# Kernel tuning notes

Measured on AMD Instinct MI355X. Metric: run time of the kernel, lower is better.

The kernel has to match this reference:

```python
import jax, jax.numpy as jnp
import numpy as np
from jax import lax

B, T, E = 2, 2048, 2048
H, D = 16, 128
C = H * D          # qk_dim == v_dim == 2048
K = 4              # short conv kernel size
EPS = 1e-5


def setup_inputs() -> dict:
    key = jax.random.key(0)
    ks = jax.random.split(key, 11)
    s = 0.02
    return {
        "x": jax.random.normal(ks[0], (B, T, E), dtype=jnp.float32),
        "recurrent_state": jnp.zeros((B, H, D, D), dtype=jnp.float32),
        "Wq": jax.random.normal(ks[1], (C, E), dtype=jnp.float32) * s,
        "Wk": jax.random.normal(ks[2], (C, E), dtype=jnp.float32) * s,
        "Wv": jax.random.normal(ks[3], (C, E), dtype=jnp.float32) * s,
        "Wbeta": jax.random.normal(ks[4], (H, E), dtype=jnp.float32) * s,
        "Wgate": jax.random.normal(ks[5], (C, E), dtype=jnp.float32) * s,
        "Wo": jax.random.normal(ks[6], (E, C), dtype=jnp.float32) * s,
        "wq_conv": jax.random.normal(ks[7], (C, 1, K), dtype=jnp.float32) * 0.5,
        "wk_conv": jax.random.normal(ks[8], (C, 1, K), dtype=jnp.float32) * 0.5,
        "wv_conv": jax.random.normal(ks[9], (C, 1, K), dtype=jnp.float32) * 0.5,
    }


def _causal_dwconv(u, w):
    # u: (B, T, C), w: (C, 1, K). Torch pads both sides by K-1 then truncates
    # to length T -> equivalent to causal left-pad of K-1.
    u = u.transpose(0, 2, 1)  # (B, C, T)
    y = lax.conv_general_dilated(
        u, w, window_strides=(1,), padding=[(K - 1, 0)],
        feature_group_count=C, dimension_numbers=("NCH", "OIH", "NCH"))
    return y.transpose(0, 2, 1)  # (B, T, C)


def _delta_scan(q, k, v, beta, state):
    # q,k,v: (B,T,H,D); beta: (B,T,H); state: (B,H,D,D)
    def step(S, inp):
        qt, kt, vt, bt = inp  # (B,H,D),(B,H,D),(B,H,D),(B,H)
        b = bt[..., None, None]
        S = (1.0 - b) * S + b * (kt[..., :, None] * vt[..., None, :])  # bhde
        o = jnp.einsum("bhde,bhd->bhe", S, qt)
        return S, o

    xs = (q.transpose(1, 0, 2, 3), k.transpose(1, 0, 2, 3),
          v.transpose(1, 0, 2, 3), beta.transpose(1, 0, 2))
    final_state, outs = lax.scan(step, state, xs)
    return outs.transpose(1, 0, 2, 3), final_state  # (B,T,H,D)


def reference(x, recurrent_state, Wq, Wk, Wv, Wbeta, Wgate, Wo,
              wq_conv, wk_conv, wv_conv):
    q = jax.nn.silu(_causal_dwconv(x @ Wq.T, wq_conv))
    k = jax.nn.silu(_causal_dwconv(x @ Wk.T, wk_conv))
    v = jax.nn.silu(_causal_dwconv(x @ Wv.T, wv_conv))
    beta = jax.nn.sigmoid(x @ Wbeta.T)   # (B,T,H)
    gate = jax.nn.sigmoid(x @ Wgate.T)   # (B,T,C)

    q = q.reshape(B, T, H, D) * (D ** -0.5)
    k = k.reshape(B, T, H, D)
    v = v.reshape(B, T, H, D)

    out, new_state = _delta_scan(q, k, v, beta, recurrent_state)  # (B,T,H,D)

    # GroupNorm(num_groups=H, channels=C, affine=False) over (B, C, T):
    # normalizes each (batch, head) group over its (D, T) elements.
    mean = out.mean(axis=(1, 3), keepdims=True)
    var = out.var(axis=(1, 3), keepdims=True)
    out = (out - mean) * lax.rsqrt(var + EPS)

    out = out.reshape(B, T, C) * gate
    y = out @ Wo.T  # (B,T,E)
    return y, new_state
```

## Files before the change

### kernel.cpp

```cpp
#include <hip/hip_runtime.h>
#include <hip/hip_bf16.h>
#include <math.h>

#define BB 2
#define TT 2048
#define EE 2048
#define HH 16
#define DD 128
#define CC 2048
#define KCONV 4
#define CHUNK 128
#define NC 16
#define GN_EPS 1e-5f

typedef __bf16 bf16x8 __attribute__((ext_vector_type(8)));
typedef __bf16 bf16x4 __attribute__((ext_vector_type(4)));
typedef float  f32x4  __attribute__((ext_vector_type(4)));

#define GLD16(gp, lp)                                                          \
  __builtin_amdgcn_global_load_lds(                                            \
      (const __attribute__((address_space(1))) void*)(gp),                     \
      (__attribute__((address_space(3))) void*)(lp), 16, 0, 0)

__device__ __forceinline__ bf16x8 ldfrag(const __bf16* buf, int row, int kg)
{
  return *(const bf16x8*)(buf + row * 128 + ((kg ^ (row & 7)) << 3));
}

__global__ __launch_bounds__(256)
void convert_w(const float* __restrict__ Wq, const float* __restrict__ Wk,
               const float* __restrict__ Wv, const float* __restrict__ Wg,
               const float* __restrict__ Wo, __bf16* __restrict__ Wcat,
               __bf16* __restrict__ Wob)
{
  const int i = (blockIdx.x * 256 + threadIdx.x) * 4;
  const int WN = 4194304;
  const float* src;
  __bf16* dst;
  int off;
  if (i < 4 * WN) {
    const int seg = i >> 22;
    src = seg == 0 ? Wq : seg == 1 ? Wk : seg == 2 ? Wv : Wg;
    dst = Wcat + ((size_t)seg << 22);
    off = i & (WN - 1);
  } else { src = Wo; dst = Wob; off = i - 4 * WN; }
  const float4 v = *(const float4*)(src + off);
  bf16x4 o;
  o[0] = (__bf16)v.x; o[1] = (__bf16)v.y; o[2] = (__bf16)v.z; o[3] = (__bf16)v.w;
  *(bf16x4*)(dst + off) = o;
}

__global__ __launch_bounds__(256)
void beta_ker(const float* __restrict__ x, const float* __restrict__ Wb,
              float* __restrict__ betab, __bf16* __restrict__ xbf)
{
  __shared__ float wsb[16 * 1024];
  const int tid = threadIdx.x;
  const int w = tid >> 6, lane = tid & 63;
  const int row = blockIdx.x * 4 + w;
  const float* xrow = x + (size_t)row * EE;
  __bf16* xbrow = xbf + (size_t)row * EE;

  float acc[16] = {};
#pragma unroll
  for (int kt = 0; kt < 2; ++kt) {
    __syncthreads();
#pragma unroll
    for (int it = 0; it < 16; ++it) {
      const int i = tid + it * 256;
      const int h = i >> 8, kq = i & 255;
      *(float4*)&wsb[h * 1024 + kq * 4] =
          *(const float4*)(Wb + (size_t)h * EE + kt * 1024 + kq * 4);
    }
    __syncthreads();
#pragma unroll
    for (int j = 0; j < 4; ++j) {
      const int kof = lane * 4 + j * 256;
      const float4 xv = *(const float4*)(xrow + kt * 1024 + kof);
      bf16x4 xb;
      xb[0] = (__bf16)xv.x; xb[1] = (__bf16)xv.y;
      xb[2] = (__bf16)xv.z; xb[3] = (__bf16)xv.w;
      *(bf16x4*)(xbrow + kt * 1024 + kof) = xb;
#pragma unroll
      for (int h = 0; h < 16; ++h) {
        const float4 wv = *(const float4*)&wsb[h * 1024 + kof];
        acc[h] += xv.x * wv.x + xv.y * wv.y + xv.z * wv.z + xv.w * wv.w;
      }
    }
  }
#pragma unroll
  for (int h = 0; h < 16; ++h) {
#pragma unroll
    for (int off = 32; off; off >>= 1)
      acc[h] += __shfl_xor(acc[h], off, 64);
  }
#pragma unroll
  for (int h = 0; h < 16; ++h)
    if (lane == h)
      betab[(size_t)row * HH + h] = 1.f / (1.f + expf(-acc[h]));
}

__global__ __launch_bounds__(512)
void gemm_big(const __bf16* __restrict__ A, const __bf16* __restrict__ Bm,
              __bf16* __restrict__ o0, __bf16* __restrict__ o1,
              __bf16* __restrict__ o2, __bf16* __restrict__ o3)
{
  __shared__ __attribute__((aligned(16))) unsigned char smem[163840];
  __bf16 (*ldsA)[256 * 64] = (__bf16(*)[256 * 64])smem;
  __bf16 (*ldsB)[256 * 64] = (__bf16(*)[256 * 64])(smem + 98304);

  const int tid = threadIdx.x;
  const int w = tid >> 6, l = tid & 63;
  const int wm = w >> 2, wn = w & 3;
  const int orig = blockIdx.x + (blockIdx.y << 5);
  const int swz = (orig & 7) * 64 + (orig >> 3);
  const int m0 = (swz & 15) * 256, n0 = (swz >> 4) * 256;
  const int NT = EE / 64;

  const int sr0 = w * 8 + (l >> 3);
  const int skg = l & 7;
  const int fr = l & 15;
  const int fkg = l >> 4;

#define STAGE_A(tile, half) do {                                               \
    const int b_ = (tile) % 3;                                                 \
    const int r0_ = sr0;                                                       \
    const int r1_ = 64 + sr0;                                                  \
    GLD16(A + (size_t)(m0 + (half) * 128 + r0_) * 2048 + (tile) * 64           \
              + ((skg ^ (r0_ & 7)) << 3),                                      \
          ldsA[b_] + ((half) * 128 + w * 8) * 64);                             \
    GLD16(A + (size_t)(m0 + (half) * 128 + r1_) * 2048 + (tile) * 64           \
              + ((skg ^ (r1_ & 7)) << 3),                                      \
          ldsA[b_] + ((half) * 128 + 64 + w * 8) * 64);                        \
  } while (0)

#define STAGE_B(tile, half) do {                                               \
    const int b_ = (tile) & 1;                                                 \
    const int r0_ = sr0;                                                       \
    const int r1_ = 64 + sr0;                                                  \
    GLD16(Bm + (size_t)(n0 + (half) * 128 + r0_) * 2048 + (tile) * 64          \
              + ((skg ^ (r0_ & 7)) << 3),                                      \
          ldsB[b_] + ((half) * 128 + w * 8) * 64);                             \
    GLD16(Bm + (size_t)(n0 + (half) * 128 + r1_) * 2048 + (tile) * 64          \
              + ((skg ^ (r1_ & 7)) << 3),                                      \
          ldsB[b_] + ((half) * 128 + 64 + w * 8) * 64);                        \
  } while (0)

#define LDA_FRAG(dst, ab, q, mf, ks) do {                                      \
    const int row_ = wm * 128 + (q) * 32 + (mf) * 16 + fr;                     \
    const int kg_ = (ks) * 4 + fkg;                                            \
    dst = *(const bf16x8*)&ldsA[ab][row_ * 64 + ((kg_ ^ (row_ & 7)) << 3)];    \
  } while (0)
#define LDB_FRAG(dst, bb, nf, ks) do {                                         \
    const int row_ = wn * 64 + (nf) * 16 + fr;                                 \
    const int kg_ = (ks) * 4 + fkg;                                            \
    dst = *(const bf16x8*)&ldsB[bb][row_ * 64 + ((kg_ ^ (row_ & 7)) << 3)];    \
  } while (0)

  f32x4 acc[8][4] = {};

  STAGE_A(0, 0); STAGE_A(0, 1); STAGE_B(0, 0); STAGE_B(0, 1);
  STAGE_A(1, 0); STAGE_A(1, 1); STAGE_B(1, 0);
  asm volatile("s_waitcnt vmcnt(6)" ::: "memory");
  __builtin_amdgcn_s_barrier();

  for (int t = 0; t < NT; ++t) {
    const int abuf = t % 3;
    const int bbuf = t & 1;
    bf16x8 bfr[4][2];

    {
      bf16x8 af[2][2];
#pragma unroll
      for (int nf = 0; nf < 4; ++nf)
#pragma unroll
        for (int ks = 0; ks < 2; ++ks) LDB_FRAG(bfr[nf][ks], bbuf, nf, ks);
#pragma unroll
      for (int mf = 0; mf < 2; ++mf)
#pragma unroll
        for (int ks = 0; ks < 2; ++ks) LDA_FRAG(af[mf][ks], abuf, 0, mf, ks);
      if (t + 1 < NT) STAGE_B(t + 1, 1);
      __builtin_amdgcn_s_barrier();
      __builtin_amdgcn_s_setprio(1);
#pragma unroll
      for (int mf = 0; mf < 2; ++mf)
#pragma unroll
        for (int nf = 0; nf < 4; ++nf)
#pragma unroll
          for (int ks = 0; ks < 2; ++ks)
            acc[mf][nf] = __builtin_amdgcn_mfma_f32_16x16x32_bf16(
                af[mf][ks], bfr[nf][ks], acc[mf][nf], 0, 0, 0);
      __builtin_amdgcn_s_setprio(0);
    }

#pragma unroll
    for (int q = 1; q < 4; ++q) {
      bf16x8 af[2][2];
#pragma unroll
      for (int mf = 0; mf < 2; ++mf)
#pragma unroll
        for (int ks = 0; ks < 2; ++ks) LDA_FRAG(af[mf][ks], abuf, q, mf, ks);
      if (q == 1) {
        if (t + 2 < NT) STAGE_A(t + 2, 0);
      } else if (q == 2) {
        if (t + 2 < NT) STAGE_A(t + 2, 1);
      } else {
        if (t + 2 < NT) STAGE_B(t + 2, 0);
        if (t == NT - 2)     asm volatile("s_waitcnt vmcnt(0)" ::: "memory");
        else if (t < NT - 2) asm volatile("s_waitcnt vmcnt(6)" ::: "memory");
      }
      __builtin_amdgcn_s_barrier();
      __builtin_amdgcn_s_setprio(1);
#pragma unroll
      for (int mf = 0; mf < 2; ++mf)
#pragma unroll
        for (int nf = 0; nf < 4; ++nf)
#pragma unroll
          for (int ks = 0; ks < 2; ++ks)
            acc[2 * q + mf][nf] = __builtin_amdgcn_mfma_f32_16x16x32_bf16(
                af[mf][ks], bfr[nf][ks], acc[2 * q + mf][nf], 0, 0, 0);
      __builtin_amdgcn_s_setprio(0);
    }
  }

  __syncthreads();
  const int proj = n0 >> 11;
  const int nb = n0 & 2047;
  __bf16* outp = proj == 0 ? o0 : proj == 1 ? o1 : proj == 2 ? o2 : o3;
  __bf16* ep = (__bf16*)smem + (size_t)w * 9216;
  const int crow = (l >> 4) * 4;
#pragma unroll
  for (int mf2 = 0; mf2 < 8; ++mf2)
#pragma unroll
    for (int nf = 0; nf < 4; ++nf)
#pragma unroll
      for (int r = 0; r < 4; ++r) {
        const int row = mf2 * 16 + crow + r;
        float vv = acc[mf2][nf][r];
        if (proj == 3) vv = 1.f / (1.f + expf(-vv));
        ep[row * 72 + nf * 16 + fr] = (__bf16)vv;
      }
#pragma unroll
  for (int it = 0; it < 16; ++it) {
    const int row = it * 8 + (l >> 3);
    const int c8 = (l & 7) * 8;
    const bf16x8 v8 = *(const bf16x8*)&ep[row * 72 + c8];
    *(bf16x8*)(outp + (size_t)(m0 + wm * 128 + row) * 2048 + nb + wn * 64 + c8) = v8;
  }
#undef STAGE_A
#undef STAGE_B
#undef LDA_FRAG
#undef LDB_FRAG
}

__global__ __launch_bounds__(512)
void gemm_wo(const __bf16* __restrict__ A, const __bf16* __restrict__ Bm,
             float* __restrict__ Cm)
{
  __shared__ __attribute__((aligned(16))) unsigned char smem[147456];
  __bf16 (*ldsA)[128 * 64] = (__bf16(*)[128 * 64])smem;
  __bf16 (*ldsB)[256 * 64] = (__bf16(*)[256 * 64])(smem + 49152);

  const int tid = threadIdx.x;
  const int w = tid >> 6, l = tid & 63;
  const int wm = w >> 2, wn = w & 3;
  const int orig = blockIdx.x + (blockIdx.y << 3);
  const int swz = (orig & 7) * 32 + (orig >> 3);
  const int m0 = (swz & 31) * 128, n0 = (swz >> 5) * 256;
  const int NT = CC / 64;

  const int sr0 = w * 8 + (l >> 3);
  const int skg = l & 7;
  const int fr = l & 15;
  const int fkg = l >> 4;

#define STAGE_AW(tile) do {                                                    \
    const int b_ = (tile) % 3;                                                 \
    const int r0_ = sr0;                                                       \
    const int r1_ = 64 + sr0;                                                  \
    GLD16(A + (size_t)(m0 + r0_) * 2048 + (tile) * 64                          \
              + ((skg ^ (r0_ & 7)) << 3),                                      \
          ldsA[b_] + (w * 8) * 64);                                            \
    GLD16(A + (size_t)(m0 + r1_) * 2048 + (tile) * 64                          \
              + ((skg ^ (r1_ & 7)) << 3),                                      \
          ldsA[b_] + (64 + w * 8) * 64);                                       \
  } while (0)

#define STAGE_BW(tile, half) do {                                              \
    const int b_ = (tile) % 3;                                                 \
    const int r0_ = sr0;                                                       \
    const int r1_ = 64 + sr0;                                                  \
    GLD16(Bm + (size_t)(n0 + (half) * 128 + r0_) * 2048 + (tile) * 64          \
              + ((skg ^ (r0_ & 7)) << 3),                                      \
          ldsB[b_] + ((half) * 128 + w * 8) * 64);                             \
    GLD16(Bm + (size_t)(n0 + (half) * 128 + r1_) * 2048 + (tile) * 64          \
              + ((skg ^ (r1_ & 7)) << 3),                                      \
          ldsB[b_] + ((half) * 128 + 64 + w * 8) * 64);                        \
  } while (0)

#define LDA_FRAGW(dst, ab, mf, ks) do {                                        \
    const int row_ = wm * 64 + (mf) * 16 + fr;                                 \
    const int kg_ = (ks) * 4 + fkg;                                            \
    dst = *(const bf16x8*)&ldsA[ab][row_ * 64 + ((kg_ ^ (row_ & 7)) << 3)];    \
  } while (0)
#define LDB_FRAGW(dst, bb, nf, ks) do {                                        \
    const int row_ = wn * 64 + (nf) * 16 + fr;                                 \
    const int kg_ = (ks) * 4 + fkg;                                            \
    dst = *(const bf16x8*)&ldsB[bb][row_ * 64 + ((kg_ ^ (row_ & 7)) << 3)];    \
  } while (0)

  f32x4 acc[4][4] = {};

  STAGE_BW(0, 0); STAGE_BW(0, 1); STAGE_AW(0);
  STAGE_BW(1, 0); STAGE_BW(1, 1); STAGE_AW(1);

  for (int t = 0; t < NT; ++t) {
    const int buf = t % 3;
    bf16x8 bfr[4][2];
    bf16x8 af[4][2];

    if (t == NT - 1) asm volatile("s_waitcnt vmcnt(0)" ::: "memory");
    else             asm volatile("s_waitcnt vmcnt(6)" ::: "memory");
    __builtin_amdgcn_s_barrier();

#pragma unroll
    for (int nf = 0; nf < 4; ++nf)
#pragma unroll
      for (int ks = 0; ks < 2; ++ks) LDB_FRAGW(bfr[nf][ks], buf, nf, ks);
#pragma unroll
    for (int mf = 0; mf < 4; ++mf)
#pragma unroll
      for (int ks = 0; ks < 2; ++ks) LDA_FRAGW(af[mf][ks], buf, mf, ks);

    if (t + 2 < NT) { STAGE_BW(t + 2, 0); STAGE_BW(t + 2, 1); STAGE_AW(t + 2); }

    __builtin_amdgcn_s_setprio(1);
#pragma unroll
    for (int mf = 0; mf < 4; ++mf)
#pragma unroll
      for (int nf = 0; nf < 4; ++nf)
#pragma unroll
        for (int ks = 0; ks < 2; ++ks)
          acc[mf][nf] = __builtin_amdgcn_mfma_f32_16x16x32_bf16(
              af[mf][ks], bfr[nf][ks], acc[mf][nf], 0, 0, 0);
    __builtin_amdgcn_s_setprio(0);
  }

  __syncthreads();
  float* ep = (float*)smem + (size_t)w * (64 * 68);
  const int crow = (l >> 4) * 4;
#pragma unroll
  for (int mf = 0; mf < 4; ++mf)
#pragma unroll
    for (int nf = 0; nf < 4; ++nf)
#pragma unroll
      for (int r = 0; r < 4; ++r)
        ep[(mf * 16 + crow + r) * 68 + nf * 16 + fr] = acc[mf][nf][r];
#pragma unroll
  for (int it = 0; it < 16; ++it) {
    const int row = it * 4 + (l >> 4);
    const int c4 = (l & 15) * 4;
    const float4 v4 = *(const float4*)&ep[row * 68 + c4];
    *(float4*)(Cm + (size_t)(m0 + wm * 64 + row) * 2048 + n0 + wn * 64 + c4) = v4;
  }
#undef STAGE_AW
#undef STAGE_BW
#undef LDA_FRAGW
#undef LDB_FRAGW
}

__global__ __launch_bounds__(256)
void conv_tr(const __bf16* __restrict__ u_q, const __bf16* __restrict__ u_k,
             const __bf16* __restrict__ u_v, const float* __restrict__ wq,
             const float* __restrict__ wk, const float* __restrict__ wv,
             __bf16* __restrict__ qbf, __bf16* __restrict__ kbf,
             __bf16* __restrict__ kT, __bf16* __restrict__ vT, float qscale)
{
  const int t0 = blockIdx.x * 64, c0 = blockIdx.y * 64;
  const int which = blockIdx.z / BB, b = blockIdx.z % BB;
  const __bf16* u = which == 0 ? u_q : which == 1 ? u_k : u_v;
  const float* wc = which == 0 ? wq : which == 1 ? wk : wv;
  const float scale = which == 0 ? qscale : 1.f;
  const int tid = threadIdx.x;
  __shared__ __attribute__((aligned(16))) __bf16 tile[64][72];

#pragma unroll
  for (int it = 0; it < 2; ++it) {
    const int idx = tid + it * 256;
    const int tl = idx >> 3, g = idx & 7;
    const int t = t0 + tl;
    const int c8 = c0 + g * 8;
    const size_t base = ((size_t)(b * TT + t)) * CC + c8;
    const bf16x8 z = {};
    const bf16x8 uu0 = *(const bf16x8*)(u + base);
    const bf16x8 uu1 = (t >= 1) ? *(const bf16x8*)(u + base - CC)     : z;
    const bf16x8 uu2 = (t >= 2) ? *(const bf16x8*)(u + base - 2 * CC) : z;
    const bf16x8 uu3 = (t >= 3) ? *(const bf16x8*)(u + base - 3 * CC) : z;
    bf16x8 o;
#pragma unroll
    for (int jj = 0; jj < 8; ++jj) {
      const float4 wv4 = *(const float4*)(wc + (size_t)(c8 + jj) * 4);
      const float vv = wv4.x * (float)uu3[jj] + wv4.y * (float)uu2[jj]
                     + wv4.z * (float)uu1[jj] + wv4.w * (float)uu0[jj];
      o[jj] = (__bf16)(vv / (1.f + expf(-vv)) * scale);
    }
    if (which == 0) *(bf16x8*)(qbf + base) = o;
    if (which == 1) *(bf16x8*)(kbf + base) = o;
    if (which >= 1) *(bf16x8*)&tile[tl][g * 8] = o;
  }
  if (which >= 1) {
    __syncthreads();
    const int h = c0 >> 7, d0 = c0 & 127;
    const int bh = b * HH + h;
    __bf16* dst = (which == 1) ? kT : vT;
#pragma unroll
    for (int it = 0; it < 2; ++it) {
      const int idx = tid + it * 256;
      const int dl = idx >> 3, g = idx & 7;
      bf16x8 o;
#pragma unroll
      for (int jj = 0; jj < 8; ++jj) o[jj] = tile[g * 8 + jj][dl];
      *(bf16x8*)(dst + ((size_t)(bh * DD + d0 + dl)) * TT + t0 + g * 8) = o;
    }
  }
}

__global__ __launch_bounds__(256)
void phaseA_mfma(const __bf16* __restrict__ kT, const __bf16* __restrict__ vT,
                 const float* __restrict__ beta, float* __restrict__ contribT,
                 float* __restrict__ decay)
{
  const int c = blockIdx.x, h = blockIdx.y, b = blockIdx.z;
  const int bh = b * HH + h;
  const int tid = threadIdx.x;
  const int w = tid >> 6, lane = tid & 63;
  const int wm = w >> 1, wn = w & 1;

  __shared__ __attribute__((aligned(16))) __bf16 bufVT[128 * 128];
  __shared__ __attribute__((aligned(16))) __bf16 bufKW[128 * 128];
  __shared__ float lc[CHUNK], bsh[CHUNK], wgt[CHUNK];

  {
    const __bf16* vbase = vT + ((size_t)bh * DD) * TT + c * CHUNK;
#pragma unroll
    for (int jj = 0; jj < 8; ++jj) {
      const int row = w * 32 + jj * 4 + (lane >> 4);
      const int g = lane & 15;
      GLD16(vbase + (size_t)row * TT + ((g ^ (row & 7)) << 3),
            bufVT + (w * 32 + jj * 4) * 128);
    }
  }

  if (tid < CHUNK) {
    const float bv = beta[(size_t)(b * TT + c * CHUNK + tid) * HH + h];
    bsh[tid] = bv;
    lc[tid] = log1pf(-bv);
  }
  __syncthreads();
  for (int off = 1; off < CHUNK; off <<= 1) {
    float add = 0.f;
    if (tid < CHUNK && tid >= off) add = lc[tid - off];
    __syncthreads();
    if (tid < CHUNK) lc[tid] += add;
    __syncthreads();
  }
  const float lend = lc[CHUNK - 1];
  if (tid < CHUNK) wgt[tid] = bsh[tid] * expf(lend - lc[tid]);
  if (tid == 0) decay[(size_t)bh * NC + c] = expf(lend);
  __syncthreads();

  {
    const __bf16* kbase = kT + ((size_t)bh * DD) * TT + c * CHUNK;
#pragma unroll
    for (int it = 0; it < 8; ++it) {
      const int idx = tid + it * 256;
      const int d = idx >> 4, g = idx & 15;
      const bf16x8 kv = *(const bf16x8*)(kbase + (size_t)d * TT + g * 8);
      bf16x8 o;
#pragma unroll
      for (int jj = 0; jj < 8; ++jj)
        o[jj] = (__bf16)((float)kv[jj] * wgt[g * 8 + jj]);
      *(bf16x8*)(bufKW + d * 128 + ((g ^ (d & 7)) << 3)) = o;
    }
  }
  asm volatile("s_waitcnt vmcnt(0)" ::: "memory");
  __syncthreads();

  f32x4 acc[4][4] = {};
#pragma unroll
  for (int ks = 0; ks < 4; ++ks) {
    bf16x8 a[4], bq[4];
    const int kg = ks * 4 + (lane >> 4);
#pragma unroll
    for (int f = 0; f < 4; ++f) a[f]  = ldfrag(bufVT, wm * 64 + f * 16 + (lane & 15), kg);
#pragma unroll
    for (int f = 0; f < 4; ++f) bq[f] = ldfrag(bufKW, wn * 64 + f * 16 + (lane & 15), kg);
#pragma unroll
    for (int i = 0; i < 4; ++i)
#pragma unroll
      for (int j = 0; j < 4; ++j)
        acc[i][j] = __builtin_amdgcn_mfma_f32_16x16x32_bf16(a[i], bq[j], acc[i][j], 0, 0, 0);
  }

  float* cp = contribT + ((size_t)(bh * NC + c) << 14);
  const int crow = (lane >> 4) * 4;
#pragma unroll
  for (int i = 0; i < 4; ++i)
#pragma unroll
    for (int j = 0; j < 4; ++j) {
      const int dd = wn * 64 + j * 16 + (lane & 15);
#pragma unroll
      for (int r = 0; r < 4; ++r) {
        const int e = wm * 64 + i * 16 + crow + r;
        cp[(size_t)e * 128 + dd] = acc[i][j][r];
      }
    }
}

__global__ __launch_bounds__(256)
void phaseB_T(const float* __restrict__ st0, const float* __restrict__ contribT,
              const float* __restrict__ decay, __bf16* __restrict__ statesT,
              float* __restrict__ stOut)
{
  const size_t gid = (size_t)blockIdx.x * 256 + threadIdx.x;
  const int bh = (int)(gid >> 14);
  const int ed = (int)(gid & 16383);
  const int e = ed >> 7, d = ed & 127;
  const size_t tidx = ((size_t)bh << 14) + (size_t)d * 128 + e;
  float s = st0[tidx];
  const float* dc = decay + (size_t)bh * NC;
#pragma unroll
  for (int c = 0; c < NC; ++c) {
    const size_t off = ((size_t)(bh * NC + c) << 14) + ed;
    statesT[off] = (__bf16)s;
    s = fmaf(dc[c], s, contribT[off]);
  }
  stOut[tidx] = s;
}

__global__ __launch_bounds__(256)
void phaseC_mfma(const __bf16* __restrict__ qb, const __bf16* __restrict__ kb,
                 const __bf16* __restrict__ vT, const float* __restrict__ beta,
                 const __bf16* __restrict__ statesT, float* __restrict__ att,
                 float* __restrict__ partials)
{
  const int c = blockIdx.x, h = blockIdx.y, b = blockIdx.z;
  const int bh = b * HH + h;
  const int tid = threadIdx.x;
  const int w = tid >> 6, lane = tid & 63;
  const int wm = w >> 1, wn = w & 1;

  __shared__ __attribute__((aligned(16))) __bf16 bufQ[128 * 128];
  __shared__ __attribute__((aligned(16))) __bf16 bufB[128 * 128];
  __shared__ float lc[CHUNK], bsh[CHUNK];
  __shared__ float s1[256], s2[256];

  {
    const __bf16* qbase = qb + ((size_t)(b * TT + c * CHUNK)) * CC + h * DD;
    const __bf16* kbase = kb + ((size_t)(b * TT + c * CHUNK)) * CC + h * DD;
#pragma unroll
    for (int jj = 0; jj < 8; ++jj) {
      const int row = w * 32 + jj * 4 + (lane >> 4);
      const int g = lane & 15;
      GLD16(qbase + (size_t)row * CC + ((g ^ (row & 7)) << 3),
            bufQ + (w * 32 + jj * 4) * 128);
      GLD16(kbase + (size_t)row * CC + ((g ^ (row & 7)) << 3),
            bufB + (w * 32 + jj * 4) * 128);
    }
  }

  if (tid < CHUNK) {
    const float bv = beta[(size_t)(b * TT + c * CHUNK + tid) * HH + h];
    bsh[tid] = bv;
    lc[tid] = log1pf(-bv);
  }
  __syncthreads();
  for (int off = 1; off < CHUNK; off <<= 1) {
    float add = 0.f;
    if (tid < CHUNK && tid >= off) add = lc[tid - off];
    __syncthreads();
    if (tid < CHUNK) lc[tid] += add;
    __syncthreads();
  }

  asm volatile("s_waitcnt vmcnt(0)" ::: "memory");
  __syncthreads();

  f32x4 accS[4][4] = {};
#pragma unroll
  for (int ks = 0; ks < 4; ++ks) {
    bf16x8 a[4], bq[4];
    const int kg = ks * 4 + (lane >> 4);
#pragma unroll
    for (int f = 0; f < 4; ++f) a[f]  = ldfrag(bufQ, wm * 64 + f * 16 + (lane & 15), kg);
#pragma unroll
    for (int f = 0; f < 4; ++f) bq[f] = ldfrag(bufB, wn * 64 + f * 16 + (lane & 15), kg);
#pragma unroll
    for (int i = 0; i < 4; ++i)
#pragma unroll
      for (int j = 0; j < 4; ++j)
        accS[i][j] = __builtin_amdgcn_mfma_f32_16x16x32_bf16(a[i], bq[j], accS[i][j], 0, 0, 0);
  }

  __syncthreads();
  {
    const __bf16* sbase = statesT + ((size_t)(bh * NC + c) << 14);
#pragma unroll
    for (int jj = 0; jj < 8; ++jj) {
      const int row = w * 32 + jj * 4 + (lane >> 4);
      const int g = lane & 15;
      GLD16(sbase + (size_t)row * 128 + ((g ^ (row & 7)) << 3),
            bufB + (w * 32 + jj * 4) * 128);
    }
  }
  asm volatile("s_waitcnt vmcnt(0)" ::: "memory");
  __syncthreads();

  f32x4 accO[4][4] = {};
#pragma unroll
  for (int ks = 0; ks < 4; ++ks) {
    bf16x8 a[4], bq[4];
    const int kg = ks * 4 + (lane >> 4);
#pragma unroll
    for (int f = 0; f < 4; ++f) a[f]  = ldfrag(bufQ, wm * 64 + f * 16 + (lane & 15), kg);
#pragma unroll
    for (int f = 0; f < 4; ++f) bq[f] = ldfrag(bufB, wn * 64 + f * 16 + (lane & 15), kg);
#pragma unroll
    for (int i = 0; i < 4; ++i)
#pragma unroll
      for (int j = 0; j < 4; ++j)
        accO[i][j] = __builtin_amdgcn_mfma_f32_16x16x32_bf16(a[i], bq[j], accO[i][j], 0, 0, 0);
  }
  const int crow = (lane >> 4) * 4;
#pragma unroll
  for (int i = 0; i < 4; ++i)
#pragma unroll
    for (int r = 0; r < 4; ++r) {
      const float el = expf(lc[wm * 64 + i * 16 + crow + r]);
#pragma unroll
      for (int j = 0; j < 4; ++j) accO[i][j][r] *= el;
    }

  __syncthreads();
  {
    const __bf16* vbase = vT + ((size_t)bh * DD) * TT + c * CHUNK;
#pragma unroll
    for (int jj = 0; jj < 8; ++jj) {
      const int row = w * 32 + jj * 4 + (lane >> 4);
      const int g = lane & 15;
      GLD16(vbase + (size_t)row * TT + ((g ^ (row & 7)) << 3),
            bufB + (w * 32 + jj * 4) * 128);
    }
  }
  {
    float lcs[4], bss[4];
#pragma unroll
    for (int j = 0; j < 4; ++j) {
      const int s = wn * 64 + j * 16 + (lane & 15);
      lcs[j] = lc[s]; bss[j] = bsh[s];
    }
#pragma unroll
    for (int i = 0; i < 4; ++i)
#pragma unroll
      for (int r = 0; r < 4; ++r) {
        const int t = wm * 64 + i * 16 + crow + r;
        const float lct = lc[t];
#pragma unroll
        for (int j = 0; j < 4; ++j) {
          const int s = wn * 64 + j * 16 + (lane & 15);
          float p = 0.f;
          if (s <= t) p = accS[i][j][r] * bss[j] * expf(lct - lcs[j]);
          bufQ[t * 128 + (((s >> 3) ^ (t & 7)) << 3) + (s & 7)] = (__bf16)p;
        }
      }
  }
  asm volatile("s_waitcnt vmcnt(0)" ::: "memory");
  __syncthreads();

#pragma unroll
  for (int ks = 0; ks < 4; ++ks) {
    bf16x8 a[4], bq[4];
    const int kg = ks * 4 + (lane >> 4);
#pragma unroll
    for (int f = 0; f < 4; ++f) a[f]  = ldfrag(bufQ, wm * 64 + f * 16 + (lane & 15), kg);
#pragma unroll
    for (int f = 0; f < 4; ++f) bq[f] = ldfrag(bufB, wn * 64 + f * 16 + (lane & 15), kg);
#pragma unroll
    for (int i = 0; i < 4; ++i)
#pragma unroll
      for (int j = 0; j < 4; ++j)
        accO[i][j] = __builtin_amdgcn_mfma_f32_16x16x32_bf16(a[i], bq[j], accO[i][j], 0, 0, 0);
  }

  float lsum = 0.f, lsq = 0.f;
  float* obase = att + ((size_t)(b * TT + c * CHUNK)) * CC + h * DD;
#pragma unroll
  for (int i = 0; i < 4; ++i)
#pragma unroll
    for (int j = 0; j < 4; ++j) {
      const int e = wn * 64 + j * 16 + (lane & 15);
#pragma unroll
      for (int r = 0; r < 4; ++r) {
        const int t = wm * 64 + i * 16 + crow + r;
        const float vv = accO[i][j][r];
        obase[(size_t)t * CC + e] = vv;
        lsum += vv;
        lsq  += vv * vv;
      }
    }
  s1[tid] = lsum; s2[tid] = lsq;
  __syncthreads();
  for (int off = 128; off; off >>= 1) {
    if (tid < off) { s1[tid] += s1[tid + off]; s2[tid] += s2[tid + off]; }
    __syncthreads();
  }
  if (tid == 0) {
    partials[(size_t)(bh * NC + c) * 2]     = s1[0];
    partials[(size_t)(bh * NC + c) * 2 + 1] = s2[0];
  }
}

__global__ __launch_bounds__(256)
void norm_gate(const float* __restrict__ att, const __bf16* __restrict__ gate,
               const float* __restrict__ partials, __bf16* __restrict__ g)
{
  __shared__ float sm[8], sr[8];
  const int tid = threadIdx.x;
  const size_t gid0 = (size_t)blockIdx.x * 1024;
  const int b = (int)(gid0 >> 22);
  const int h0 = ((int)(gid0 & 2047)) >> 7;
  if (tid < 8) {
    const int bh = b * HH + h0 + tid;
    float s = 0.f, q = 0.f;
#pragma unroll
    for (int cc = 0; cc < NC; ++cc) {
      s += partials[(size_t)(bh * NC + cc) * 2];
      q += partials[(size_t)(bh * NC + cc) * 2 + 1];
    }
    const float n = (float)(TT * DD);
    const float mean = s / n;
    sm[tid] = mean;
    sr[tid] = rsqrtf(q / n - mean * mean + GN_EPS);
  }
  __syncthreads();
  const size_t gid = gid0 + (size_t)tid * 4;
  const int hl = (tid * 4) >> 7;
  const float mean = sm[hl], rstd = sr[hl];
  const float4 a = *(const float4*)(att + gid);
  const bf16x4 gt = *(const bf16x4*)(gate + gid);
  bf16x4 o;
  o[0] = (__bf16)((a.x - mean) * rstd * (float)gt[0]);
  o[1] = (__bf16)((a.y - mean) * rstd * (float)gt[1]);
  o[2] = (__bf16)((a.z - mean) * rstd * (float)gt[2]);
  o[3] = (__bf16)((a.w - mean) * rstd * (float)gt[3]);
  *(bf16x4*)(g + gid) = o;
}

extern "C" void kernel_launch(void* const* d_in, const int* in_sizes, int n_in,
                              void* d_out, int out_size, void* d_ws, size_t ws_size,
                              hipStream_t stream)
{
  const float* x      = (const float*)d_in[0];
  const float* st0    = (const float*)d_in[1];
  const float* Wq     = (const float*)d_in[2];
  const float* Wk     = (const float*)d_in[3];
  const float* Wv     = (const float*)d_in[4];
  const float* Wbeta  = (const float*)d_in[5];
  const float* Wgate  = (const float*)d_in[6];
  const float* Wo     = (const float*)d_in[7];
  const float* wqc    = (const float*)d_in[8];
  const float* wkc    = (const float*)d_in[9];
  const float* wvc    = (const float*)d_in[10];

  float* ws = (float*)d_ws;
  __bf16* qbf  = (__bf16*)(ws + 0);
  __bf16* kbf  = (__bf16*)(ws + 4194304);
  __bf16* u_v  = (__bf16*)(ws + 8388608);
  __bf16* statesT = (__bf16*)(ws + 8388608);
  __bf16* kT   = (__bf16*)(ws + 12582912);
  __bf16* gbf  = (__bf16*)(ws + 12582912);
  __bf16* vT   = (__bf16*)(ws + 16777216);
  __bf16* xbf  = (__bf16*)(ws + 20971520);
  float* contribT = ws + 20971520;
  __bf16* Wcat = (__bf16*)(ws + 25165824);
  __bf16* gatebuf = (__bf16*)(ws + 33554432);
  float* betab    = ws + 37748736;
  float* decay    = ws + 37814272;
  float* partials = ws + 37814848;
  __bf16* Wob  = (__bf16*)(ws + 38864448);

  float* y_out  = (float*)d_out;
  float* st_out = (float*)d_out + (size_t)BB * TT * EE;
  __bf16* u_q = (__bf16*)d_out;
  __bf16* u_k = (__bf16*)d_out + 8388608;
  float* att = y_out;

  const dim3 blk(256);
  const dim3 gBig(8192 / 256, (BB * TT) / 256);
  const dim3 gWo(EE / 256, (BB * TT) / 128);
  const dim3 gConv(TT / 64, CC / 64, 3 * BB);
  const dim3 gScan(NC, HH, BB);
  const float qscale = 0.08838834764831845f;

  convert_w<<<dim3(20480), blk, 0, stream>>>(Wq, Wk, Wv, Wgate, Wo, Wcat, Wob);

  beta_ker<<<dim3((BB * TT) / 4), blk, 0, stream>>>(x, Wbeta, betab, xbf);

  gemm_big<<<gBig, dim3(512), 0, stream>>>(xbf, Wcat, u_q, u_k, u_v, gatebuf);

  conv_tr<<<gConv, blk, 0, stream>>>(u_q, u_k, u_v, wqc, wkc, wvc,
                                     qbf, kbf, kT, vT, qscale);

  phaseA_mfma<<<gScan, blk, 0, stream>>>(kT, vT, betab, contribT, decay);
  phaseB_T<<<dim3((BB * HH * DD * DD) / 256), blk, 0, stream>>>(st0, contribT, decay, statesT, st_out);
  phaseC_mfma<<<gScan, blk, 0, stream>>>(qbf, kbf, vT, betab, statesT, att, partials);

  norm_gate<<<dim3((BB * TT * CC) / 1024), blk, 0, stream>>>(att, gatebuf, partials, gbf);

  gemm_wo<<<gWo, dim3(512), 0, stream>>>(gbf, Wob, y_out);
}
```

Measured before the change: 334.8 us.

## Hold Q fragments in registers and co-load K and state in phaseC

In phaseC, each wave now loads its Q fragments straight from global memory into registers, which frees an LDS buffer. K and the chunk state can then be staged together in one batch of async loads, removing a barrier and a serial load/wait step between the QK^T and Q·S matmuls. Separately, the GEMM kernels drop their block-index swizzle in favour of direct blockIdx mapping, which may change L2 reuse. Holding 16 bf16x8 Q fragments adds register pressure, and the Q loads are strided global reads rather than async LDS copies.

Result: no change. 328.8 us (-1.8%).

```diff
diff --git a/kernel.cpp b/kernel.cpp
--- a/kernel.cpp
+++ b/kernel.cpp
@@ -112,9 +112,7 @@
   const int tid = threadIdx.x;
   const int w = tid >> 6, l = tid & 63;
   const int wm = w >> 2, wn = w & 3;
-  const int orig = blockIdx.x + (blockIdx.y << 5);
-  const int swz = (orig & 7) * 64 + (orig >> 3);
-  const int m0 = (swz & 15) * 256, n0 = (swz >> 4) * 256;
+  const int m0 = blockIdx.y * 256, n0 = blockIdx.x * 256;
   const int NT = EE / 64;
 
   const int sr0 = w * 8 + (l >> 3);
@@ -264,9 +262,7 @@
   const int tid = threadIdx.x;
   const int w = tid >> 6, l = tid & 63;
   const int wm = w >> 2, wn = w & 3;
-  const int orig = blockIdx.x + (blockIdx.y << 3);
-  const int swz = (orig & 7) * 32 + (orig >> 3);
-  const int m0 = (swz & 31) * 128, n0 = (swz >> 5) * 256;
+  const int m0 = blockIdx.y * 128, n0 = blockIdx.x * 256;
   const int NT = CC / 64;
 
   const int sr0 = w * 8 + (l >> 3);
@@ -550,21 +546,32 @@
   const int w = tid >> 6, lane = tid & 63;
   const int wm = w >> 1, wn = w & 1;
 
-  __shared__ __attribute__((aligned(16))) __bf16 bufQ[128 * 128];
+  __shared__ __attribute__((aligned(16))) __bf16 bufA[128 * 128];
   __shared__ __attribute__((aligned(16))) __bf16 bufB[128 * 128];
   __shared__ float lc[CHUNK], bsh[CHUNK];
   __shared__ float s1[256], s2[256];
 
+  bf16x8 qf[4][4];
   {
-    const __bf16* qbase = qb + ((size_t)(b * TT + c * CHUNK)) * CC + h * DD;
+    const __bf16* qbase = qb + ((size_t)(b * TT + c * CHUNK + wm * 64 + (lane & 15))) * CC
+                        + h * DD + (lane >> 4) * 8;
+#pragma unroll
+    for (int f = 0; f < 4; ++f)
+#pragma unroll
+      for (int ks = 0; ks < 4; ++ks)
+        qf[f][ks] = *(const bf16x8*)(qbase + (size_t)f * 16 * CC + ks * 32);
+  }
+
+  {
     const __bf16* kbase = kb + ((size_t)(b * TT + c * CHUNK)) * CC + h * DD;
+    const __bf16* sbase = statesT + ((size_t)(bh * NC + c) << 14);
 #pragma unroll
     for (int jj = 0; jj < 8; ++jj) {
       const int row = w * 32 + jj * 4 + (lane >> 4);
       const int g = lane & 15;
-      GLD16(qbase + (size_t)row * CC + ((g ^ (row & 7)) << 3),
-            bufQ + (w * 32 + jj * 4) * 128);
       GLD16(kbase + (size_t)row * CC + ((g ^ (row & 7)) << 3),
+            bufA + (w * 32 + jj * 4) * 128);
+      GLD16(sbase + (size_t)row * 128 + ((g ^ (row & 7)) << 3),
             bufB + (w * 32 + jj * 4) * 128);
     }
   }
@@ -589,47 +596,29 @@
   f32x4 accS[4][4] = {};
 #pragma unroll
   for (int ks = 0; ks < 4; ++ks) {
-    bf16x8 a[4], bq[4];
+    bf16x8 bq[4];
     const int kg = ks * 4 + (lane >> 4);
 #pragma unroll
-    for (int f = 0; f < 4; ++f) a[f]  = ldfrag(bufQ, wm * 64 + f * 16 + (lane & 15), kg);
+    for (int f = 0; f < 4; ++f) bq[f] = ldfrag(bufA, wn * 64 + f * 16 + (lane & 15), kg);
+#pragma unroll
+    for (int i = 0; i < 4; ++i)
+#pragma unroll
+      for (int j = 0; j < 4; ++j)
+        accS[i][j] = __builtin_amdgcn_mfma_f32_16x16x32_bf16(qf[i][ks], bq[j], accS[i][j], 0, 0, 0);
+  }
+
+  f32x4 accO[4][4] = {};
+#pragma unroll
+  for (int ks = 0; ks < 4; ++ks) {
+    bf16x8 bq[4];
+    const int kg = ks * 4 + (lane >> 4);
 #pragma unroll
     for (int f = 0; f < 4; ++f) bq[f] = ldfrag(bufB, wn * 64 + f * 16 + (lane & 15), kg);
 #pragma unroll
     for (int i = 0; i < 4; ++i)
 #pragma unroll
       for (int j = 0; j < 4; ++j)
-        accS[i][j] = __builtin_amdgcn_mfma_f32_16x16x32_bf16(a[i], bq[j], accS[i][j], 0, 0, 0);
-  }
-
-  __syncthreads();
-  {
-    const __bf16* sbase = statesT + ((size_t)(bh * NC + c) << 14);
-#pragma unroll
-    for (int jj = 0; jj < 8; ++jj) {
-      const int row = w * 32 + jj * 4 + (lane >> 4);
-      const int g = lane & 15;
-      GLD16(sbase + (size_t)row * 128 + ((g ^ (row & 7)) << 3),
-            bufB + (w * 32 + jj * 4) * 128);
-    }
-  }
-  asm volatile("s_waitcnt vmcnt(0)" ::: "memory");
-  __syncthreads();
-
-  f32x4 accO[4][4] = {};
-#pragma unroll
-  for (int ks = 0; ks < 4; ++ks) {
-    bf16x8 a[4], bq[4];
-    const int kg = ks * 4 + (lane >> 4);
-#pragma unroll
-    for (int f = 0; f < 4; ++f) a[f]  = ldfrag(bufQ, wm * 64 + f * 16 + (lane & 15), kg);
-#pragma unroll
-    for (int f = 0; f < 4; ++f) bq[f] = ldfrag(bufB, wn * 64 + f * 16 + (lane & 15), kg);
-#pragma unroll
-    for (int i = 0; i < 4; ++i)
-#pragma unroll
-      for (int j = 0; j < 4; ++j)
-        accO[i][j] = __builtin_amdgcn_mfma_f32_16x16x32_bf16(a[i], bq[j], accO[i][j], 0, 0, 0);
+        accO[i][j] = __builtin_amdgcn_mfma_f32_16x16x32_bf16(qf[i][ks], bq[j], accO[i][j], 0, 0, 0);
   }
   const int crow = (lane >> 4) * 4;
 #pragma unroll
@@ -642,6 +631,7 @@
     }
 
   __syncthreads();
+
   {
     const __bf16* vbase = vT + ((size_t)bh * DD) * TT + c * CHUNK;
 #pragma unroll
@@ -670,7 +660,7 @@
           const int s = wn * 64 + j * 16 + (lane & 15);
           float p = 0.f;
           if (s <= t) p = accS[i][j][r] * bss[j] * expf(lct - lcs[j]);
-          bufQ[t * 128 + (((s >> 3) ^ (t & 7)) << 3) + (s & 7)] = (__bf16)p;
+          bufA[t * 128 + (((s >> 3) ^ (t & 7)) << 3) + (s & 7)] = (__bf16)p;
         }
       }
   }
@@ -682,7 +672,7 @@
     bf16x8 a[4], bq[4];
     const int kg = ks * 4 + (lane >> 4);
 #pragma unroll
-    for (int f = 0; f < 4; ++f) a[f]  = ldfrag(bufQ, wm * 64 + f * 16 + (lane & 15), kg);
+    for (int f = 0; f < 4; ++f) a[f]  = ldfrag(bufA, wm * 64 + f * 16 + (lane & 15), kg);
 #pragma unroll
     for (int f = 0; f < 4; ++f) bq[f] = ldfrag(bufB, wn * 64 + f * 16 + (lane & 15), kg);
 #pragma unroll
```
